# Performance work log

Measured on AMD Instinct MI355X. Metric: run time of the kernel, lower is better.

## Reference

```python
import jax, jax.numpy as jnp
import numpy as np

B, S, D = 2, 4096, 2048
H = 16
DC = 512       # dim_c
DKQV = 2048    # dim_kqv
DR = 1024      # dim_r
DCKV = 512     # dim_c_kv
DOUT = 2048
DH = DKQV // H   # 128
DRH = DR // H    # 64
SCALER = 1.0 / float(np.sqrt(DH + DRH))


def _rope(x):
    # x: [B, S, H, DRH]; rotation indexed by sequence position (axis 1)
    dr = x.shape[-1]
    inv_freq = 1.0 / (10000.0 ** (jnp.arange(0, dr, 2, dtype=jnp.float32) / dr))
    t = jnp.arange(x.shape[1], dtype=jnp.float32)
    freqs = t[:, None] * inv_freq[None, :]            # [S, dr/2]
    emb = jnp.concatenate([freqs, freqs], axis=-1)[None, :, None, :]  # [1,S,1,dr]
    x1, x2 = jnp.split(x, 2, axis=-1)
    rot = jnp.concatenate([-x2, x1], axis=-1)
    return x * jnp.cos(emb) + rot * jnp.sin(emb)


def setup_inputs() -> dict:
    key = jax.random.key(0)
    ks = jax.random.split(key, 20)
    def lin(k, din, dout):
        s = 1.0 / np.sqrt(din)
        kw, kb = jax.random.split(k)
        W = jax.random.uniform(kw, (din, dout), jnp.float32, -s, s)
        b = jax.random.uniform(kb, (dout,), jnp.float32, -s, s)
        return W, b
    h_t = jax.random.normal(ks[0], (B, S, D), jnp.float32)
    Wc, bc = lin(ks[1], D, DC)
    Wcq, bcq = lin(ks[2], DC, DKQV)
    Wqr, bqr = lin(ks[3], DC, DR)
    Wckv, bckv = lin(ks[4], D, DCKV)
    Wck, bck = lin(ks[5], DCKV, DKQV)
    Wkr, bkr = lin(ks[6], D, DR)
    Wv, bv = lin(ks[7], DCKV, DKQV)
    Wo, bo = lin(ks[8], DKQV, DOUT)
    return dict(h_t=h_t, Wc=Wc, bc=bc, Wcq=Wcq, bcq=bcq, Wqr=Wqr, bqr=bqr,
                Wckv=Wckv, bckv=bckv, Wck=Wck, bck=bck, Wkr=Wkr, bkr=bkr,
                Wv=Wv, bv=bv, Wo=Wo, bo=bo)


def reference(h_t, Wc, bc, Wcq, bcq, Wqr, bqr, Wckv, bckv, Wck, bck,
              Wkr, bkr, Wv, bv, Wo, bo):
    b, s = h_t.shape[0], h_t.shape[1]
    cq = h_t @ Wc + bc                                   # [B,S,DC]
    q = (cq @ Wcq + bcq).reshape(b, s, H, DH)            # [B,S,H,DH]
    qr = _rope((cq @ Wqr + bqr).reshape(b, s, H, DRH))   # [B,S,H,DRH]
    q = jnp.concatenate([q, qr], axis=-1)                # [B,S,H,DH+DRH]
    ckv = h_t @ Wckv + bckv                              # [B,S,DCKV]
    k = (ckv @ Wck + bck).reshape(b, s, H, DH)
    kr = _rope((h_t @ Wkr + bkr).reshape(b, s, H, DRH))
    k = jnp.concatenate([k, kr], axis=-1)
    v = (ckv @ Wv + bv).reshape(b, s, H, DH)
    # Faithful to source: matmul over last two dims of [B,S,H,d] ->
    # per-position head-vs-head scores [B,S,H,H], softmax over heads.
    scores = jnp.einsum('bsid,bsjd->bsij', q, k) * SCALER
    attn = jax.nn.softmax(scores, axis=-1)
    out = jnp.einsum('bsij,bsjd->bsid', attn, v).reshape(b, s, DKQV)
    return out @ Wo + bo
```

## Files before the change

### kernel.cpp

```cpp
#include <hip/hip_runtime.h>
#include <hip/hip_bf16.h>
#include <stdint.h>


typedef __bf16 bf16_t;
typedef __bf16 bf16x8 __attribute__((ext_vector_type(8)));
typedef float f32x4 __attribute__((ext_vector_type(4)));

__device__ __forceinline__ void async_copy16(const void* g, void* l) {
  __builtin_amdgcn_global_load_lds(
      (__attribute__((address_space(1))) void*)(void*)g,
      (__attribute__((address_space(3))) void*)l, 16, 0, 0);
}

template <typename OT>
__global__ __launch_bounds__(512, 2) void gemm_bt256(
    const bf16_t* __restrict__ A, long lda,
    const bf16_t* __restrict__ BT,
    const float* __restrict__ bias,
    OT* __restrict__ C, long ldc,
    int M, int N, int K)
{
  __shared__ __align__(16) bf16_t As[4][8192];
  __shared__ __align__(16) bf16_t Bs[4][8192];

  const int tid  = threadIdx.x;
  const int lane = tid & 63;
  const int w    = tid >> 6;
  const int wm   = w >> 2, wn = w & 3;
  const int quad = lane >> 4, r16 = lane & 15;
  const long row0 = (long)blockIdx.y * 256;
  const long col0 = (long)blockIdx.x * 256;
  const int NT = K >> 5;

  const int rr0 = tid >> 2;
  const int cg0 = (((tid & 3) ^ (rr0 & 3)) << 3);

  f32x4 acc[8][4];
#pragma unroll
  for (int i = 0; i < 8; i++)
#pragma unroll
    for (int j = 0; j < 4; j++)
      acc[i][j] = (f32x4){0.f, 0.f, 0.f, 0.f};

#pragma unroll
  for (int t = 0; t < 3; t++) {
    const long kk = (long)((t < NT) ? t : NT - 1) << 5;
    const long ga = (row0 + rr0) * lda + kk + cg0;
    const long gb = (col0 + rr0) * (long)K + kk + cg0;
    async_copy16(A  + ga,                  &As[t][w * 512]);
    async_copy16(BT + gb,                  &Bs[t][w * 512]);
    async_copy16(A  + ga + 128 * lda,      &As[t][4096 + w * 512]);
    async_copy16(BT + gb + 128 * (long)K,  &Bs[t][4096 + w * 512]);
  }
  asm volatile("s_waitcnt vmcnt(8)" ::: "memory");
  __builtin_amdgcn_s_barrier();

  for (int t = 0; t < NT; t++) {
    const bf16_t* as = &As[t & 3][0];
    const bf16_t* bs = &Bs[t & 3][0];
    bf16_t* pa = &As[(t + 3) & 3][0];
    bf16_t* pb = &Bs[(t + 3) & 3][0];
    const int  pt  = ((t + 3) < NT) ? (t + 3) : NT - 1;
    const long pkk = (long)pt << 5;
    const long ga = (row0 + rr0) * lda + pkk + cg0;
    const long gb = (col0 + rr0) * (long)K + pkk + cg0;

    bf16x8 av[4], bv[4];

#pragma unroll
    for (int i = 0; i < 4; i++) {
      const int ra = wm * 128 + i * 16 + r16;
      av[i] = *(const bf16x8*)(as + ra * 32 + ((quad ^ (ra & 3)) << 3));
    }
#pragma unroll
    for (int j = 0; j < 4; j++) {
      const int rb = wn * 64 + j * 16 + r16;
      bv[j] = *(const bf16x8*)(bs + rb * 32 + ((quad ^ (rb & 3)) << 3));
    }
    async_copy16(A  + ga, pa + w * 512);
    async_copy16(BT + gb, pb + w * 512);
    asm volatile("" ::: "memory");
    __builtin_amdgcn_s_barrier();
    asm volatile("s_waitcnt lgkmcnt(0)" ::: "memory");
    __builtin_amdgcn_sched_barrier(0);
    __builtin_amdgcn_s_setprio(1);
#pragma unroll
    for (int i = 0; i < 4; i++)
#pragma unroll
      for (int j = 0; j < 4; j++)
        acc[i][j] = __builtin_amdgcn_mfma_f32_16x16x32_bf16(av[i], bv[j], acc[i][j], 0, 0, 0);
    __builtin_amdgcn_s_setprio(0);
    __builtin_amdgcn_sched_barrier(0);
    asm volatile("" ::: "memory");
    __builtin_amdgcn_s_barrier();

#pragma unroll
    for (int i = 0; i < 4; i++) {
      const int ra = wm * 128 + 64 + i * 16 + r16;
      av[i] = *(const bf16x8*)(as + ra * 32 + ((quad ^ (ra & 3)) << 3));
    }
    async_copy16(A  + ga + 128 * lda,     pa + 4096 + w * 512);
    async_copy16(BT + gb + 128 * (long)K, pb + 4096 + w * 512);
    asm volatile("" ::: "memory");
    __builtin_amdgcn_s_barrier();
    asm volatile("s_waitcnt lgkmcnt(0)" ::: "memory");
    __builtin_amdgcn_sched_barrier(0);
    __builtin_amdgcn_s_setprio(1);
#pragma unroll
    for (int i = 0; i < 4; i++)
#pragma unroll
      for (int j = 0; j < 4; j++)
        acc[i + 4][j] = __builtin_amdgcn_mfma_f32_16x16x32_bf16(av[i], bv[j], acc[i + 4][j], 0, 0, 0);
    __builtin_amdgcn_s_setprio(0);
    asm volatile("s_waitcnt vmcnt(8)" ::: "memory");
    __builtin_amdgcn_sched_barrier(0);
    asm volatile("" ::: "memory");
    __builtin_amdgcn_s_barrier();
  }

#pragma unroll
  for (int j = 0; j < 4; j++) {
    const float bj = bias[col0 + wn * 64 + j * 16 + r16];
#pragma unroll
    for (int i = 0; i < 8; i++) {
      acc[i][j][0] += bj; acc[i][j][1] += bj;
      acc[i][j][2] += bj; acc[i][j][3] += bj;
    }
  }

  if constexpr (sizeof(OT) == 2) {
    asm volatile("s_waitcnt vmcnt(0)" ::: "memory");
    __builtin_amdgcn_s_barrier();
    bf16_t* wreg = (w < 4) ? &As[w][0] : &Bs[w - 4][0];
#pragma unroll
    for (int i = 0; i < 8; i++)
#pragma unroll
      for (int j = 0; j < 4; j++)
#pragma unroll
        for (int r = 0; r < 4; r++)
          wreg[(i * 16 + quad * 4 + r) * 64 + j * 16 + r16] = (bf16_t)acc[i][j][r];
    asm volatile("s_waitcnt lgkmcnt(0)" ::: "memory");
    __builtin_amdgcn_s_barrier();
#pragma unroll
    for (int it = 0; it < 16; it++) {
      const int r = it * 16 + (tid >> 5);
      const int c = (tid & 31) * 8;
      const int ww = ((r >> 7) << 2) + (c >> 6);
      const bf16_t* src = ((ww < 4) ? &As[ww][0] : &Bs[ww - 4][0])
                          + (r & 127) * 64 + (c & 63);
      *(bf16x8*)((bf16_t*)C + (row0 + r) * ldc + col0 + c) = *(const bf16x8*)src;
    }
  } else {
#pragma unroll
    for (int j = 0; j < 4; j++) {
      const long col = col0 + wn * 64 + j * 16 + r16;
#pragma unroll
      for (int i = 0; i < 8; i++) {
        const long row = row0 + wm * 128 + i * 16 + quad * 4;
#pragma unroll
        for (int r = 0; r < 4; r++)
          C[(row + r) * ldc + col] = (OT)acc[i][j][r];
      }
    }
  }
}

__global__ void transpose_f32_bf16(const float* __restrict__ in, bf16_t* __restrict__ out,
                                   int R, int C)
{
  __shared__ bf16_t tile[32][33];
  const int cb = blockIdx.x * 32, rb = blockIdx.y * 32;
  const int tx = threadIdx.x, ty = threadIdx.y;
#pragma unroll
  for (int i = 0; i < 32; i += 8)
    tile[ty + i][tx] = (bf16_t)in[(size_t)(rb + ty + i) * C + cb + tx];
  __syncthreads();
#pragma unroll
  for (int i = 0; i < 32; i += 8)
    out[(size_t)(cb + ty + i) * R + rb + tx] = tile[tx][ty + i];
}

__global__ void cvt_f32_bf16(const float* __restrict__ in, bf16_t* __restrict__ out, long n)
{
  const long i = ((long)blockIdx.x * blockDim.x + threadIdx.x) * 8;
  if (i >= n) return;
  const float4 a = *(const float4*)(in + i);
  const float4 b = *(const float4*)(in + i + 4);
  bf16x8 o;
  o[0] = (bf16_t)a.x; o[1] = (bf16_t)a.y; o[2] = (bf16_t)a.z; o[3] = (bf16_t)a.w;
  o[4] = (bf16_t)b.x; o[5] = (bf16_t)b.y; o[6] = (bf16_t)b.z; o[7] = (bf16_t)b.w;
  *(bf16x8*)(out + i) = o;
}

__global__ void concat_bias(const float* bc, const float* bckv, const float* bkr,
                            const float* bcq, const float* bqr,
                            const float* bck, const float* bv,
                            float* b1, float* b2, float* b3)
{
  const int t = blockIdx.x * 256 + threadIdx.x;
  if (t < 2048) {
    b1[t] = (t < 512) ? bc[t] : (t < 1024) ? bckv[t - 512] : bkr[t - 1024];
  } else if (t < 5120) {
    const int u = t - 2048;
    b2[u] = (u < 2048) ? bcq[u] : bqr[u - 2048];
  } else if (t < 9216) {
    const int u = t - 5120;
    b3[u] = (u < 2048) ? bck[u] : bv[u - 2048];
  }
}

__global__ __launch_bounds__(256) void attn_rope(
    const bf16_t* __restrict__ f1, bf16_t* f2, const bf16_t* __restrict__ f3)
{
  const int tok = blockIdx.x;
  const int pos = tok & 4095;
  const int tid = threadIdx.x;

  __shared__ __align__(16) float qf[16 * 204];
  __shared__ __align__(16) float kf[16 * 204];
  __shared__ __align__(16) float vf[16 * 132];
  __shared__ float sc[256];

  const bf16_t* q  = f2 + (size_t)tok * 3072;
  const bf16_t* qr = q + 2048;
  const bf16_t* k  = f3 + (size_t)tok * 4096;
  const bf16_t* v  = k + 2048;
  const bf16_t* kr = f1 + (size_t)tok * 2048 + 1024;

  {
    const int h = tid >> 4, d = (tid & 15) * 8;
    bf16x8 xq = *(const bf16x8*)(q + tid * 8);
    bf16x8 xk = *(const bf16x8*)(k + tid * 8);
    bf16x8 xv = *(const bf16x8*)(v + tid * 8);
    float* qd = qf + h * 204 + d;
    float* kd = kf + h * 204 + d;
    float* vd = vf + h * 132 + d;
#pragma unroll
    for (int e = 0; e < 8; e++) {
      qd[e] = (float)xq[e];
      kd[e] = (float)xk[e];
      vd[e] = (float)xv[e];
    }
  }

  for (int p = tid; p < 512; p += 256) {
    const int h = p >> 5, j = p & 31;
    const float x1 = (float)qr[h * 64 + j];
    const float x2 = (float)qr[h * 64 + j + 32];
    const float y1 = (float)kr[h * 64 + j];
    const float y2 = (float)kr[h * 64 + j + 32];
    const float ang = (float)pos * exp2f((float)j * -0.41524101186092029f);
    float sn, cs;
    sincosf(ang, &sn, &cs);
    qf[h * 204 + 128 + j] = x1 * cs - x2 * sn;
    qf[h * 204 + 160 + j] = x2 * cs + x1 * sn;
    kf[h * 204 + 128 + j] = y1 * cs - y2 * sn;
    kf[h * 204 + 160 + j] = y2 * cs + y1 * sn;
  }
  __syncthreads();

  {
    const int i = tid >> 4, j = tid & 15;
    const float4* qrow = (const float4*)(qf + i * 204);
    const float4* krow = (const float4*)(kf + j * 204);
    float d0 = 0.f, d1 = 0.f, d2 = 0.f, d3 = 0.f;
#pragma unroll 8
    for (int dd = 0; dd < 48; dd++) {
      const float4 a = qrow[dd], b = krow[dd];
      d0 = fmaf(a.x, b.x, d0);
      d1 = fmaf(a.y, b.y, d1);
      d2 = fmaf(a.z, b.z, d2);
      d3 = fmaf(a.w, b.w, d3);
    }
    const float s = (d0 + d1 + d2 + d3) * 0.07216878364870323f;
    float m = s;
    m = fmaxf(m, __shfl_xor(m, 1));
    m = fmaxf(m, __shfl_xor(m, 2));
    m = fmaxf(m, __shfl_xor(m, 4));
    m = fmaxf(m, __shfl_xor(m, 8));
    const float e = __expf(s - m);
    float sum = e;
    sum += __shfl_xor(sum, 1);
    sum += __shfl_xor(sum, 2);
    sum += __shfl_xor(sum, 4);
    sum += __shfl_xor(sum, 8);
    sc[i * 16 + j] = e / sum;
  }
  __syncthreads();

  {
    const int i = tid >> 4, dp = (tid & 15) * 8;
    float4 a0 = {0.f, 0.f, 0.f, 0.f}, a1 = {0.f, 0.f, 0.f, 0.f};
#pragma unroll
    for (int j = 0; j < 16; j++) {
      const float a = sc[i * 16 + j];
      const float4* vrow = (const float4*)(vf + j * 132 + dp);
      const float4 v0 = vrow[0], v1 = vrow[1];
      a0.x = fmaf(a, v0.x, a0.x);
      a0.y = fmaf(a, v0.y, a0.y);
      a0.z = fmaf(a, v0.z, a0.z);
      a0.w = fmaf(a, v0.w, a0.w);
      a1.x = fmaf(a, v1.x, a1.x);
      a1.y = fmaf(a, v1.y, a1.y);
      a1.z = fmaf(a, v1.z, a1.z);
      a1.w = fmaf(a, v1.w, a1.w);
    }
    bf16x8 o;
    o[0] = (bf16_t)a0.x; o[1] = (bf16_t)a0.y; o[2] = (bf16_t)a0.z; o[3] = (bf16_t)a0.w;
    o[4] = (bf16_t)a1.x; o[5] = (bf16_t)a1.y; o[6] = (bf16_t)a1.z; o[7] = (bf16_t)a1.w;
    *(bf16x8*)(f2 + (size_t)tok * 3072 + i * 128 + dp) = o;
  }
}

extern "C" void kernel_launch(void* const* d_in, const int* in_sizes, int n_in,
                              void* d_out, int out_size, void* d_ws, size_t ws_size,
                              hipStream_t stream)
{
  (void)in_sizes; (void)n_in; (void)out_size; (void)ws_size;

  const float* h_t  = (const float*)d_in[0];
  const float* Wc   = (const float*)d_in[1];
  const float* bc   = (const float*)d_in[2];
  const float* Wcq  = (const float*)d_in[3];
  const float* bcq  = (const float*)d_in[4];
  const float* Wqr  = (const float*)d_in[5];
  const float* bqr  = (const float*)d_in[6];
  const float* Wckv = (const float*)d_in[7];
  const float* bckv = (const float*)d_in[8];
  const float* Wck  = (const float*)d_in[9];
  const float* bck  = (const float*)d_in[10];
  const float* Wkr  = (const float*)d_in[11];
  const float* bkr  = (const float*)d_in[12];
  const float* Wv   = (const float*)d_in[13];
  const float* bv   = (const float*)d_in[14];
  const float* Wo   = (const float*)d_in[15];
  const float* bo   = (const float*)d_in[16];

  bf16_t* ws = (bf16_t*)d_ws;
  bf16_t* W1T    = ws + 0;
  bf16_t* W2T    = ws + 4194304;
  bf16_t* W3T    = ws + 5767168;
  bf16_t* WoT    = ws + 7864320;
  bf16_t* fused1 = ws + 12058624;
  bf16_t* fused2 = ws + 28835840;
  bf16_t* fused3 = ws + 54001664;

  bf16_t* hbf = (bf16_t*)d_out;
  float*  b1  = (float*)((char*)d_out + 33554432);
  float*  b2  = b1 + 2048;
  float*  b3  = b2 + 3072;

  const dim3 tb(32, 8);
  transpose_f32_bf16<<<dim3(16, 64), tb, 0, stream>>>(Wc,   W1T,                2048, 512);
  transpose_f32_bf16<<<dim3(16, 64), tb, 0, stream>>>(Wckv, W1T + 512  * 2048,  2048, 512);
  transpose_f32_bf16<<<dim3(32, 64), tb, 0, stream>>>(Wkr,  W1T + 1024 * 2048,  2048, 1024);
  transpose_f32_bf16<<<dim3(64, 16), tb, 0, stream>>>(Wcq,  W2T,                512, 2048);
  transpose_f32_bf16<<<dim3(32, 16), tb, 0, stream>>>(Wqr,  W2T + 2048 * 512,   512, 1024);
  transpose_f32_bf16<<<dim3(64, 16), tb, 0, stream>>>(Wck,  W3T,                512, 2048);
  transpose_f32_bf16<<<dim3(64, 16), tb, 0, stream>>>(Wv,   W3T + 2048 * 512,   512, 2048);
  transpose_f32_bf16<<<dim3(64, 64), tb, 0, stream>>>(Wo,   WoT,                2048, 2048);
  concat_bias<<<36, 256, 0, stream>>>(bc, bckv, bkr, bcq, bqr, bck, bv, b1, b2, b3);
  cvt_f32_bf16<<<8192, 256, 0, stream>>>(h_t, hbf, 16777216L);

  gemm_bt256<bf16_t><<<dim3(8, 32), 512, 0, stream>>>(hbf, 2048, W1T, b1, fused1, 2048, 8192, 2048, 2048);
  gemm_bt256<bf16_t><<<dim3(12, 32), 512, 0, stream>>>(fused1, 2048, W2T, b2, fused2, 3072, 8192, 3072, 512);
  gemm_bt256<bf16_t><<<dim3(16, 32), 512, 0, stream>>>(fused1 + 512, 2048, W3T, b3, fused3, 4096, 8192, 4096, 512);

  attn_rope<<<8192, 256, 0, stream>>>(fused1, fused2, fused3);

  gemm_bt256<float><<<dim3(8, 32), 512, 0, stream>>>(fused2, 3072, WoT, bo, (float*)d_out, 2048, 8192, 2048, 2048);
}
```

Before: 505.6 us.

## Double-buffer GEMM with K=64 stages and per-16-row subtile LDS layout

Replaces the 4-deep ring of K=32 LDS stages with two K=64 buffers, each split into two K=32 halves that are refilled in turn as the main loop consumes them. LDS tiles are reorganised into contiguous 16-row by 32-column subtiles with an XOR swizzle on the read and write offsets, so each MFMA operand fetch reads one contiguous 1KB block. The aim is to halve loop iterations and barrier overhead per K and to cut LDS bank conflicts. Prefetch now runs less far ahead of compute, and the vmcnt accounting and buffer reuse in the epilogue must stay consistent with the new staging order.

Result: slower. 551.7 us (+9.1%).

```diff
diff --git a/kernel.cpp b/kernel.cpp
--- a/kernel.cpp
+++ b/kernel.cpp
@@ -21,8 +21,8 @@
     OT* __restrict__ C, long ldc,
     int M, int N, int K)
 {
-  __shared__ __align__(16) bf16_t As[4][8192];
-  __shared__ __align__(16) bf16_t Bs[4][8192];
+  __shared__ __align__(16) bf16_t As[2][16384];
+  __shared__ __align__(16) bf16_t Bs[2][16384];
 
   const int tid  = threadIdx.x;
   const int lane = tid & 63;
@@ -31,10 +31,24 @@
   const int quad = lane >> 4, r16 = lane & 15;
   const long row0 = (long)blockIdx.y * 256;
   const long col0 = (long)blockIdx.x * 256;
-  const int NT = K >> 5;
-
-  const int rr0 = tid >> 2;
-  const int cg0 = (((tid & 3) ^ (rr0 & 3)) << 3);
+  const int NT = K >> 6;
+
+  const bf16_t* Ab = A + row0 * lda;
+  const bf16_t* Bb = BT + col0 * (long)K;
+
+  const int rdoff = r16 * 32 + ((quad * 8) ^ ((r16 & 8) ? 16 : 0));
+
+  const int srin = lane >> 2;
+  const int sksw = ((lane & 3) * 8) ^ ((lane & 32) ? 16 : 0);
+
+  auto stage = [&](const bf16_t* G, long ld, bf16_t* dstOp, int Kc) {
+#pragma unroll
+    for (int s = 0; s < 2; s++) {
+      const int m = s * 8 + w;
+      async_copy16(G + (long)(m * 16 + srin) * ld + Kc * 32 + sksw,
+                   dstOp + ((m * 2 + Kc) << 9));
+    }
+  };
 
   f32x4 acc[8][4];
 #pragma unroll
@@ -43,43 +57,37 @@
     for (int j = 0; j < 4; j++)
       acc[i][j] = (f32x4){0.f, 0.f, 0.f, 0.f};
 
-#pragma unroll
-  for (int t = 0; t < 3; t++) {
-    const long kk = (long)((t < NT) ? t : NT - 1) << 5;
-    const long ga = (row0 + rr0) * lda + kk + cg0;
-    const long gb = (col0 + rr0) * (long)K + kk + cg0;
-    async_copy16(A  + ga,                  &As[t][w * 512]);
-    async_copy16(BT + gb,                  &Bs[t][w * 512]);
-    async_copy16(A  + ga + 128 * lda,      &As[t][4096 + w * 512]);
-    async_copy16(BT + gb + 128 * (long)K,  &Bs[t][4096 + w * 512]);
+  {
+    const long k1 = (long)((1 < NT) ? 1 : NT - 1) << 6;
+    stage(Ab, lda, As[0], 0);
+    stage(Bb, K,   Bs[0], 0);
+    stage(Ab, lda, As[0], 1);
+    stage(Bb, K,   Bs[0], 1);
+    stage(Ab + k1, lda, As[1], 0);
+    stage(Bb + k1, K,   Bs[1], 0);
   }
   asm volatile("s_waitcnt vmcnt(8)" ::: "memory");
   __builtin_amdgcn_s_barrier();
 
   for (int t = 0; t < NT; t++) {
-    const bf16_t* as = &As[t & 3][0];
-    const bf16_t* bs = &Bs[t & 3][0];
-    bf16_t* pa = &As[(t + 3) & 3][0];
-    bf16_t* pb = &Bs[(t + 3) & 3][0];
-    const int  pt  = ((t + 3) < NT) ? (t + 3) : NT - 1;
-    const long pkk = (long)pt << 5;
-    const long ga = (row0 + rr0) * lda + pkk + cg0;
-    const long gb = (col0 + rr0) * (long)K + pkk + cg0;
+    const bf16_t* a0 = As[t & 1];
+    const bf16_t* b0 = Bs[t & 1];
+    bf16_t* an = As[(t + 1) & 1];
+    bf16_t* bn = Bs[(t + 1) & 1];
+    bf16_t* ac = As[t & 1];
+    bf16_t* bc = Bs[t & 1];
+    const long k1 = (long)((t + 1 < NT) ? t + 1 : NT - 1) << 6;
+    const long k2 = (long)((t + 2 < NT) ? t + 2 : NT - 1) << 6;
 
     bf16x8 av[4], bv[4];
 
 #pragma unroll
-    for (int i = 0; i < 4; i++) {
-      const int ra = wm * 128 + i * 16 + r16;
-      av[i] = *(const bf16x8*)(as + ra * 32 + ((quad ^ (ra & 3)) << 3));
-    }
-#pragma unroll
-    for (int j = 0; j < 4; j++) {
-      const int rb = wn * 64 + j * 16 + r16;
-      bv[j] = *(const bf16x8*)(bs + rb * 32 + ((quad ^ (rb & 3)) << 3));
-    }
-    async_copy16(A  + ga, pa + w * 512);
-    async_copy16(BT + gb, pb + w * 512);
+    for (int i = 0; i < 4; i++)
+      av[i] = *(const bf16x8*)(a0 + (((wm * 8 + i) * 2 + 0) << 9) + rdoff);
+#pragma unroll
+    for (int j = 0; j < 4; j++)
+      bv[j] = *(const bf16x8*)(b0 + (((wn * 4 + j) * 2 + 0) << 9) + rdoff);
+    stage(Ab + k1, lda, an, 1);
     asm volatile("" ::: "memory");
     __builtin_amdgcn_s_barrier();
     asm volatile("s_waitcnt lgkmcnt(0)" ::: "memory");
@@ -96,12 +104,9 @@
     __builtin_amdgcn_s_barrier();
 
 #pragma unroll
-    for (int i = 0; i < 4; i++) {
-      const int ra = wm * 128 + 64 + i * 16 + r16;
-      av[i] = *(const bf16x8*)(as + ra * 32 + ((quad ^ (ra & 3)) << 3));
-    }
-    async_copy16(A  + ga + 128 * lda,     pa + 4096 + w * 512);
-    async_copy16(BT + gb + 128 * (long)K, pb + 4096 + w * 512);
+    for (int i = 0; i < 4; i++)
+      av[i] = *(const bf16x8*)(a0 + (((wm * 8 + 4 + i) * 2 + 0) << 9) + rdoff);
+    stage(Bb + k1, K, bn, 1);
     asm volatile("" ::: "memory");
     __builtin_amdgcn_s_barrier();
     asm volatile("s_waitcnt lgkmcnt(0)" ::: "memory");
@@ -111,13 +116,58 @@
     for (int i = 0; i < 4; i++)
 #pragma unroll
       for (int j = 0; j < 4; j++)
-        acc[i + 4][j] = __builtin_amdgcn_mfma_f32_16x16x32_bf16(av[i], bv[j], acc[i + 4][j], 0, 0, 0);
+        acc[4 + i][j] = __builtin_amdgcn_mfma_f32_16x16x32_bf16(av[i], bv[j], acc[4 + i][j], 0, 0, 0);
     __builtin_amdgcn_s_setprio(0);
     asm volatile("s_waitcnt vmcnt(8)" ::: "memory");
     __builtin_amdgcn_sched_barrier(0);
     asm volatile("" ::: "memory");
     __builtin_amdgcn_s_barrier();
-  }
+
+#pragma unroll
+    for (int i = 0; i < 4; i++)
+      av[i] = *(const bf16x8*)(a0 + (((wm * 8 + i) * 2 + 1) << 9) + rdoff);
+#pragma unroll
+    for (int j = 0; j < 4; j++)
+      bv[j] = *(const bf16x8*)(b0 + (((wn * 4 + j) * 2 + 1) << 9) + rdoff);
+    stage(Ab + k2, lda, ac, 0);
+    asm volatile("" ::: "memory");
+    __builtin_amdgcn_s_barrier();
+    asm volatile("s_waitcnt lgkmcnt(0)" ::: "memory");
+    __builtin_amdgcn_sched_barrier(0);
+    __builtin_amdgcn_s_setprio(1);
+#pragma unroll
+    for (int i = 0; i < 4; i++)
+#pragma unroll
+      for (int j = 0; j < 4; j++)
+        acc[i][j] = __builtin_amdgcn_mfma_f32_16x16x32_bf16(av[i], bv[j], acc[i][j], 0, 0, 0);
+    __builtin_amdgcn_s_setprio(0);
+    __builtin_amdgcn_sched_barrier(0);
+    asm volatile("" ::: "memory");
+    __builtin_amdgcn_s_barrier();
+
+#pragma unroll
+    for (int i = 0; i < 4; i++)
+      av[i] = *(const bf16x8*)(a0 + (((wm * 8 + 4 + i) * 2 + 1) << 9) + rdoff);
+    stage(Bb + k2, K, bc, 0);
+    asm volatile("" ::: "memory");
+    __builtin_amdgcn_s_barrier();
+    asm volatile("s_waitcnt lgkmcnt(0)" ::: "memory");
+    __builtin_amdgcn_sched_barrier(0);
+    __builtin_amdgcn_s_setprio(1);
+#pragma unroll
+    for (int i = 0; i < 4; i++)
+#pragma unroll
+      for (int j = 0; j < 4; j++)
+        acc[4 + i][j] = __builtin_amdgcn_mfma_f32_16x16x32_bf16(av[i], bv[j], acc[4 + i][j], 0, 0, 0);
+    __builtin_amdgcn_s_setprio(0);
+    asm volatile("s_waitcnt vmcnt(8)" ::: "memory");
+    __builtin_amdgcn_sched_barrier(0);
+    asm volatile("" ::: "memory");
+    __builtin_amdgcn_s_barrier();
+  }
+
+  asm volatile("s_waitcnt vmcnt(0)" ::: "memory");
+  __builtin_amdgcn_s_barrier();
 
 #pragma unroll
   for (int j = 0; j < 4; j++) {
@@ -130,9 +180,8 @@
   }
 
   if constexpr (sizeof(OT) == 2) {
-    asm volatile("s_waitcnt vmcnt(0)" ::: "memory");
-    __builtin_amdgcn_s_barrier();
-    bf16_t* wreg = (w < 4) ? &As[w][0] : &Bs[w - 4][0];
+    bf16_t* wreg = (w < 4) ? &As[w >> 1][(w & 1) * 8192]
+                           : &Bs[(w - 4) >> 1][((w - 4) & 1) * 8192];
 #pragma unroll
     for (int i = 0; i < 8; i++)
 #pragma unroll
@@ -147,7 +196,8 @@
       const int r = it * 16 + (tid >> 5);
       const int c = (tid & 31) * 8;
       const int ww = ((r >> 7) << 2) + (c >> 6);
-      const bf16_t* src = ((ww < 4) ? &As[ww][0] : &Bs[ww - 4][0])
+      const bf16_t* src = ((ww < 4) ? &As[ww >> 1][(ww & 1) * 8192]
+                                    : &Bs[(ww - 4) >> 1][((ww - 4) & 1) * 8192])
                           + (r & 127) * 64 + (c & 63);
       *(bf16x8*)((bf16_t*)C + (row0 + r) * ldc + col0 + c) = *(const bf16x8*)src;
     }
```
